# Optimization experiments

Measured on AMD Instinct MI355X. Metric: run time of the kernel, lower is better.

Reference implementation:

```python
import jax, jax.numpy as jnp
import numpy as np

N, C, H, W = 8, 21, 512, 512
POWER = 1
EPS = 1e-8

def setup_inputs() -> dict:
    key = jax.random.key(0)
    k1, k2 = jax.random.split(key)
    inp = jax.random.normal(k1, (N, C, H, W), dtype=jnp.float32)
    tgt = jax.random.normal(k2, (N, C, H, W), dtype=jnp.float32)
    return {"input": inp, "target": tgt}

def reference(input, target):
    n, c, h, w = input.shape
    # target.argmax(1) -> one-hot mask (to_one_hot with clamp; argmax already in [0, c-1])
    labels = jnp.argmax(target, axis=1)                      # [n, h, w]
    ymask = jax.nn.one_hot(labels, c, axis=1, dtype=input.dtype)  # [n, c, h, w]

    log_p = jax.nn.log_softmax(input, axis=1)
    p = jax.nn.softmax(input, axis=1)

    # lambda_mat is None -> zf_dict: lamb[i][j] = 0.5 for all i, j
    lamb = jnp.full((c, c), 0.5, dtype=input.dtype)

    # Per-class pixel counts n_i and pairwise sums S[i, j] = sum(p[:, i] * ymask[:, j])
    counts = ymask.sum(axis=(0, 2, 3))                       # [c]
    S = jnp.einsum('nihw,njhw->ij', p, ymask)                # [c, c]

    safe_counts = jnp.where(counts > 0, counts, 1.0)
    diag = jnp.diagonal(S)                                   # S[i, i]
    # mcc.sum() for pair (i, j) = S[i,i]/n_i - S[i,j]/n_j
    mcc_sum = diag[:, None] / safe_counts[:, None] - S / safe_counts[None, :]

    term = -lamb * jnp.log((0.5 * mcc_sum + 0.5) ** POWER + EPS)
    valid = (counts[:, None] > 0) & (counts[None, :] > 0) & (~jnp.eye(c, dtype=bool))
    lossd = jnp.where(valid, term, 0.0).sum()

    # weight is None -> ymask1 == ymask
    logpy = (log_p * ymask).sum(axis=1)                      # [n, h, w]
    loss = -logpy.mean()
    return loss + lossd
```

## Files before the change

### kernel.cpp

```cpp
#include <hip/hip_runtime.h>

#define BLOCK 256
#define GRID 1024

namespace {
constexpr int C = 21;
constexpr int HW = 512 * 512;
constexpr int NPIX = 8 * HW;
constexpr int NGRP = NPIX / 4;
constexpr int CH4 = HW / 4;
constexpr float EPS = 1e-8f;
constexpr int WS_S = 0;
constexpr int WS_CNT = C * C;
constexpr int WS_LOGP = C * C + C;
constexpr int WS_FLOATS = C * C + C + 1;
}

__global__ __launch_bounds__(BLOCK) void wce_main(const float* __restrict__ inp,
                                                  const float* __restrict__ tgt,
                                                  float* __restrict__ acc) {
    __shared__ float sS[C * C];
    __shared__ float sCnt[C];
    __shared__ float sRed[BLOCK / 64];

    const int tid = threadIdx.x;
    for (int i = tid; i < C * C; i += BLOCK) sS[i] = 0.f;
    if (tid < C) sCnt[tid] = 0.f;
    __syncthreads();

    float logpy_acc = 0.f;

    for (int g = blockIdx.x * BLOCK + tid; g < NGRP; g += GRID * BLOCK) {
        const int pix0 = g << 2;
        const int n = pix0 >> 18;
        const int hw = pix0 & (HW - 1);
        const unsigned base = (unsigned)n * (unsigned)(C * HW) + (unsigned)hw;

        const float4* tp = reinterpret_cast<const float4*>(tgt + base);
        float4 bv = tp[0];
        int bx = 0, by = 0, bz = 0, bw = 0;
#pragma unroll
        for (int c = 1; c < C; ++c) {
            const float4 t = tp[c * CH4];
            if (t.x > bv.x) { bv.x = t.x; bx = c; }
            if (t.y > bv.y) { bv.y = t.y; by = c; }
            if (t.z > bv.z) { bv.z = t.z; bz = c; }
            if (t.w > bv.w) { bv.w = t.w; bw = c; }
        }

        const float4* ip = reinterpret_cast<const float4*>(inp + base);
        float4 x[C];
        x[0] = ip[0];
        float4 m = x[0];
        float4 xlab = x[0];
#pragma unroll
        for (int c = 1; c < C; ++c) {
            x[c] = ip[c * CH4];
            m.x = fmaxf(m.x, x[c].x);
            m.y = fmaxf(m.y, x[c].y);
            m.z = fmaxf(m.z, x[c].z);
            m.w = fmaxf(m.w, x[c].w);
            if (bx == c) xlab.x = x[c].x;
            if (by == c) xlab.y = x[c].y;
            if (bz == c) xlab.z = x[c].z;
            if (bw == c) xlab.w = x[c].w;
        }

        float4 s = make_float4(0.f, 0.f, 0.f, 0.f);
#pragma unroll
        for (int c = 0; c < C; ++c) {
            float4 e;
            e.x = __expf(x[c].x - m.x);
            e.y = __expf(x[c].y - m.y);
            e.z = __expf(x[c].z - m.z);
            e.w = __expf(x[c].w - m.w);
            s.x += e.x; s.y += e.y; s.z += e.z; s.w += e.w;
            x[c] = e;
        }

        logpy_acc += (xlab.x - m.x - __logf(s.x))
                   + (xlab.y - m.y - __logf(s.y))
                   + (xlab.z - m.z - __logf(s.z))
                   + (xlab.w - m.w - __logf(s.w));

        const float ix = 1.f / s.x, iy = 1.f / s.y, iz = 1.f / s.z, iw = 1.f / s.w;
#pragma unroll
        for (int c = 0; c < C; ++c) {
            unsafeAtomicAdd(&sS[c * C + bx], x[c].x * ix);
            unsafeAtomicAdd(&sS[c * C + by], x[c].y * iy);
            unsafeAtomicAdd(&sS[c * C + bz], x[c].z * iz);
            unsafeAtomicAdd(&sS[c * C + bw], x[c].w * iw);
        }
        unsafeAtomicAdd(&sCnt[bx], 1.f);
        unsafeAtomicAdd(&sCnt[by], 1.f);
        unsafeAtomicAdd(&sCnt[bz], 1.f);
        unsafeAtomicAdd(&sCnt[bw], 1.f);
    }

#pragma unroll
    for (int off = 32; off > 0; off >>= 1) logpy_acc += __shfl_down(logpy_acc, off);
    if ((tid & 63) == 0) sRed[tid >> 6] = logpy_acc;
    __syncthreads();

    if (tid == 0) {
        float t = 0.f;
        for (int wv = 0; wv < BLOCK / 64; ++wv) t += sRed[wv];
        unsafeAtomicAdd(&acc[WS_LOGP], t);
    }
    for (int i = tid; i < C * C; i += BLOCK) unsafeAtomicAdd(&acc[WS_S + i], sS[i]);
    if (tid < C) unsafeAtomicAdd(&acc[WS_CNT + tid], sCnt[tid]);
}

__global__ void wce_final(const float* __restrict__ acc, float* __restrict__ out) {
    __shared__ float cnts[C];
    __shared__ float red[8];
    const int tid = threadIdx.x;
    if (tid < C) cnts[tid] = acc[WS_CNT + tid];
    __syncthreads();

    float partial = 0.f;
    if (tid < C * C) {
        const int i = tid / C;
        const int j = tid - i * C;
        if (i != j) {
            const float ci = cnts[i], cj = cnts[j];
            if (ci > 0.f && cj > 0.f) {
                const float mcc = acc[WS_S + i * C + i] / ci - acc[WS_S + i * C + j] / cj;
                partial = -0.5f * __logf(0.5f * mcc + 0.5f + EPS);
            }
        }
    }
#pragma unroll
    for (int off = 32; off > 0; off >>= 1) partial += __shfl_down(partial, off);
    if ((tid & 63) == 0) red[tid >> 6] = partial;
    __syncthreads();

    if (tid == 0) {
        float lossd = 0.f;
        for (int wv = 0; wv < 512 / 64; ++wv) lossd += red[wv];
        const float loss = -acc[WS_LOGP] / (float)NPIX;
        out[0] = loss + lossd;
    }
}

extern "C" void kernel_launch(void* const* d_in, const int* in_sizes, int n_in,
                              void* d_out, int out_size, void* d_ws, size_t ws_size,
                              hipStream_t stream) {
    const float* inp = (const float*)d_in[0];
    const float* tgt = (const float*)d_in[1];
    float* acc = (float*)d_ws;
    float* out = (float*)d_out;

    hipMemsetAsync(acc, 0, WS_FLOATS * sizeof(float), stream);
    wce_main<<<GRID, BLOCK, 0, stream>>>(inp, tgt, acc);
    wce_final<<<1, 512, 0, stream>>>(acc, out);
}
```

Measured before the change: 276.5 us.

## Map one pixel per thread and spread global atomics over replicated accumulators

Drops the grid-stride loop that handled four pixels per thread with float4 loads. The new layout launches one thread per pixel, with 4096 blocks of 512 threads. Each block's shared-memory partials are added into one of up to 64 replicated global accumulator copies, chosen by block index, and the final kernel sums the copies. This is meant to raise occupancy and memory parallelism and to cut contention on global atomics. The cost is more blocks, so more flushes of the shared histogram, scalar loads instead of vector loads, and a larger memset.

```diff
diff --git a/kernel.cpp b/kernel.cpp
--- a/kernel.cpp
+++ b/kernel.cpp
@@ -1,24 +1,24 @@
 #include <hip/hip_runtime.h>
 
-#define BLOCK 256
-#define GRID 1024
+#define BLOCK 512
+#define GRID 4096
 
 namespace {
 constexpr int C = 21;
 constexpr int HW = 512 * 512;
 constexpr int NPIX = 8 * HW;
-constexpr int NGRP = NPIX / 4;
-constexpr int CH4 = HW / 4;
 constexpr float EPS = 1e-8f;
-constexpr int WS_S = 0;
 constexpr int WS_CNT = C * C;
 constexpr int WS_LOGP = C * C + C;
-constexpr int WS_FLOATS = C * C + C + 1;
+constexpr int ACC_USED = C * C + C + 1;
+constexpr int ACC_STRIDE = 464;
+constexpr int MAX_COPIES = 64;
 }
 
 __global__ __launch_bounds__(BLOCK) void wce_main(const float* __restrict__ inp,
                                                   const float* __restrict__ tgt,
-                                                  float* __restrict__ acc) {
+                                                  float* __restrict__ acc,
+                                                  int copy_mask) {
     __shared__ float sS[C * C];
     __shared__ float sCnt[C];
     __shared__ float sRed[BLOCK / 64];
@@ -28,94 +28,71 @@
     if (tid < C) sCnt[tid] = 0.f;
     __syncthreads();
 
-    float logpy_acc = 0.f;
+    const int px = blockIdx.x * BLOCK + tid;
+    const int n = px >> 18;
+    const int hw = px & (HW - 1);
+    const size_t base = (size_t)n * (size_t)(C * HW) + (size_t)hw;
+    const float* __restrict__ tp = tgt + base;
+    const float* __restrict__ ip = inp + base;
 
-    for (int g = blockIdx.x * BLOCK + tid; g < NGRP; g += GRID * BLOCK) {
-        const int pix0 = g << 2;
-        const int n = pix0 >> 18;
-        const int hw = pix0 & (HW - 1);
-        const unsigned base = (unsigned)n * (unsigned)(C * HW) + (unsigned)hw;
-
-        const float4* tp = reinterpret_cast<const float4*>(tgt + base);
-        float4 bv = tp[0];
-        int bx = 0, by = 0, bz = 0, bw = 0;
+    float bv = tp[0];
+    int lab = 0;
 #pragma unroll
-        for (int c = 1; c < C; ++c) {
-            const float4 t = tp[c * CH4];
-            if (t.x > bv.x) { bv.x = t.x; bx = c; }
-            if (t.y > bv.y) { bv.y = t.y; by = c; }
-            if (t.z > bv.z) { bv.z = t.z; bz = c; }
-            if (t.w > bv.w) { bv.w = t.w; bw = c; }
-        }
-
-        const float4* ip = reinterpret_cast<const float4*>(inp + base);
-        float4 x[C];
-        x[0] = ip[0];
-        float4 m = x[0];
-        float4 xlab = x[0];
-#pragma unroll
-        for (int c = 1; c < C; ++c) {
-            x[c] = ip[c * CH4];
-            m.x = fmaxf(m.x, x[c].x);
-            m.y = fmaxf(m.y, x[c].y);
-            m.z = fmaxf(m.z, x[c].z);
-            m.w = fmaxf(m.w, x[c].w);
-            if (bx == c) xlab.x = x[c].x;
-            if (by == c) xlab.y = x[c].y;
-            if (bz == c) xlab.z = x[c].z;
-            if (bw == c) xlab.w = x[c].w;
-        }
-
-        float4 s = make_float4(0.f, 0.f, 0.f, 0.f);
-#pragma unroll
-        for (int c = 0; c < C; ++c) {
-            float4 e;
-            e.x = __expf(x[c].x - m.x);
-            e.y = __expf(x[c].y - m.y);
-            e.z = __expf(x[c].z - m.z);
-            e.w = __expf(x[c].w - m.w);
-            s.x += e.x; s.y += e.y; s.z += e.z; s.w += e.w;
-            x[c] = e;
-        }
-
-        logpy_acc += (xlab.x - m.x - __logf(s.x))
-                   + (xlab.y - m.y - __logf(s.y))
-                   + (xlab.z - m.z - __logf(s.z))
-                   + (xlab.w - m.w - __logf(s.w));
-
-        const float ix = 1.f / s.x, iy = 1.f / s.y, iz = 1.f / s.z, iw = 1.f / s.w;
-#pragma unroll
-        for (int c = 0; c < C; ++c) {
-            unsafeAtomicAdd(&sS[c * C + bx], x[c].x * ix);
-            unsafeAtomicAdd(&sS[c * C + by], x[c].y * iy);
-            unsafeAtomicAdd(&sS[c * C + bz], x[c].z * iz);
-            unsafeAtomicAdd(&sS[c * C + bw], x[c].w * iw);
-        }
-        unsafeAtomicAdd(&sCnt[bx], 1.f);
-        unsafeAtomicAdd(&sCnt[by], 1.f);
-        unsafeAtomicAdd(&sCnt[bz], 1.f);
-        unsafeAtomicAdd(&sCnt[bw], 1.f);
+    for (int c = 1; c < C; ++c) {
+        const float v = tp[c * HW];
+        if (v > bv) { bv = v; lab = c; }
     }
 
+    float x[C];
 #pragma unroll
-    for (int off = 32; off > 0; off >>= 1) logpy_acc += __shfl_down(logpy_acc, off);
-    if ((tid & 63) == 0) sRed[tid >> 6] = logpy_acc;
+    for (int c = 0; c < C; ++c) x[c] = ip[c * HW];
+    float m = x[0];
+#pragma unroll
+    for (int c = 1; c < C; ++c) m = fmaxf(m, x[c]);
+
+    float xlab = x[0];
+#pragma unroll
+    for (int c = 1; c < C; ++c) if (lab == c) xlab = x[c];
+
+    float s = 0.f;
+#pragma unroll
+    for (int c = 0; c < C; ++c) { x[c] = __expf(x[c] - m); s += x[c]; }
+
+    const float logpy = xlab - m - __logf(s);
+
+    const float inv = 1.f / s;
+#pragma unroll
+    for (int c = 0; c < C; ++c) unsafeAtomicAdd(&sS[c * C + lab], x[c] * inv);
+    unsafeAtomicAdd(&sCnt[lab], 1.f);
+
+    float lp = logpy;
+#pragma unroll
+    for (int off = 32; off > 0; off >>= 1) lp += __shfl_down(lp, off);
+    if ((tid & 63) == 0) sRed[tid >> 6] = lp;
     __syncthreads();
 
+    float* __restrict__ a = acc + (size_t)(blockIdx.x & copy_mask) * ACC_STRIDE;
+    for (int i = tid; i < C * C; i += BLOCK) unsafeAtomicAdd(&a[i], sS[i]);
+    if (tid < C) unsafeAtomicAdd(&a[WS_CNT + tid], sCnt[tid]);
     if (tid == 0) {
         float t = 0.f;
+#pragma unroll
         for (int wv = 0; wv < BLOCK / 64; ++wv) t += sRed[wv];
-        unsafeAtomicAdd(&acc[WS_LOGP], t);
+        unsafeAtomicAdd(&a[WS_LOGP], t);
     }
-    for (int i = tid; i < C * C; i += BLOCK) unsafeAtomicAdd(&acc[WS_S + i], sS[i]);
-    if (tid < C) unsafeAtomicAdd(&acc[WS_CNT + tid], sCnt[tid]);
 }
 
-__global__ void wce_final(const float* __restrict__ acc, float* __restrict__ out) {
-    __shared__ float cnts[C];
+__global__ void wce_final(const float* __restrict__ acc, float* __restrict__ out,
+                          int copies) {
+    __shared__ float tot[ACC_USED];
     __shared__ float red[8];
     const int tid = threadIdx.x;
-    if (tid < C) cnts[tid] = acc[WS_CNT + tid];
+
+    for (int i = tid; i < ACC_USED; i += 512) {
+        float s = 0.f;
+        for (int k = 0; k < copies; ++k) s += acc[(size_t)k * ACC_STRIDE + i];
+        tot[i] = s;
+    }
     __syncthreads();
 
     float partial = 0.f;
@@ -123,9 +100,9 @@
         const int i = tid / C;
         const int j = tid - i * C;
         if (i != j) {
-            const float ci = cnts[i], cj = cnts[j];
+            const float ci = tot[WS_CNT + i], cj = tot[WS_CNT + j];
             if (ci > 0.f && cj > 0.f) {
-                const float mcc = acc[WS_S + i * C + i] / ci - acc[WS_S + i * C + j] / cj;
+                const float mcc = tot[i * C + i] / ci - tot[i * C + j] / cj;
                 partial = -0.5f * __logf(0.5f * mcc + 0.5f + EPS);
             }
         }
@@ -137,8 +114,9 @@
 
     if (tid == 0) {
         float lossd = 0.f;
-        for (int wv = 0; wv < 512 / 64; ++wv) lossd += red[wv];
-        const float loss = -acc[WS_LOGP] / (float)NPIX;
+#pragma unroll
+        for (int wv = 0; wv < 8; ++wv) lossd += red[wv];
+        const float loss = -tot[WS_LOGP] / (float)NPIX;
         out[0] = loss + lossd;
     }
 }
@@ -151,7 +129,11 @@
     float* acc = (float*)d_ws;
     float* out = (float*)d_out;
 
-    hipMemsetAsync(acc, 0, WS_FLOATS * sizeof(float), stream);
-    wce_main<<<GRID, BLOCK, 0, stream>>>(inp, tgt, acc);
-    wce_final<<<1, 512, 0, stream>>>(acc, out);
+    int copies = 1;
+    const size_t per = (size_t)ACC_STRIDE * sizeof(float);
+    while (copies * 2 <= MAX_COPIES && (size_t)(copies * 2) * per <= ws_size) copies *= 2;
+
+    hipMemsetAsync(acc, 0, (size_t)copies * per, stream);
+    wce_main<<<GRID, BLOCK, 0, stream>>>(inp, tgt, acc, copies - 1);
+    wce_final<<<1, 512, 0, stream>>>(acc, out, copies);
 }
```

New measurement: 272.5 us. No clear change (-1.4%).
